# Performance work log

Measured on AMD Instinct MI355X. Metric: run time of the kernel, lower is better.

The kernel has to match this reference:

```python
import jax, jax.numpy as jnp
import numpy as np

B, C, N = 8, 256, 4096
K = C // 4  # projection dim for F and G (feat_dim // 4)


def setup_inputs() -> dict:
    key = jax.random.key(0)
    k1, k2, k3, k4, k5, k6 = jax.random.split(key, 6)
    inp = {
        "input": jax.random.normal(k1, (B, C, N), dtype=jnp.float32),
        "nms_feat": jax.random.normal(k2, (B, C, N), dtype=jnp.float32),
        "WF": jax.random.normal(k3, (K, C), dtype=jnp.float32) * (1.0 / np.sqrt(C)),
        "WG": jax.random.normal(k4, (K, C), dtype=jnp.float32) * (1.0 / np.sqrt(C)),
        "WH": jax.random.normal(k5, (C, C), dtype=jnp.float32) * (1.0 / np.sqrt(C)),
        "gamma": jax.random.normal(k6, (1,), dtype=jnp.float32),
    }
    return inp


def reference(input, nms_feat, WF, WG, WH, gamma):
    feat = nms_feat  # [B, C, N]; module uses nms_feat when provided
    b, c, n = feat.shape
    # 1x1 conv projections == channel matmuls; outputs laid out as [B, N, d]
    f = jnp.einsum('kc,bcn->bnk', WF, feat)   # [B, N, K]
    g = jnp.einsum('kc,bcn->bnk', WG, feat)   # [B, N, K]
    h = jnp.einsum('dc,bcn->bnd', WH, feat)   # [B, N, C]
    # attention scores (no scaling in original module)
    s = jnp.einsum('bnk,bmk->bnm', g, f)      # [B, N, N]
    beta = jax.nn.softmax(s, axis=-1)
    o = jnp.einsum('bnm,bmd->bnd', beta, h)   # [B, N, C]
    # NOTE: the original does a raw reshape [B,N,C] -> [B,C,N] (not a transpose);
    # we reproduce that exactly.
    o = o.reshape(b, c, n)
    return gamma * o + input
```

## Files before the change

kernel.cpp:

```cpp
#include <hip/hip_runtime.h>
#include <hip/hip_bf16.h>

#define BB 8
#define CC 256
#define NN 4096
#define KP 64
#define LOG2E 1.44269504088896f

typedef _Float16 f16x8 __attribute__((ext_vector_type(8)));
typedef _Float16 f16x4 __attribute__((ext_vector_type(4)));
typedef float    f32x4 __attribute__((ext_vector_type(4)));

#define MFMA16(a, b, c) __builtin_amdgcn_mfma_f32_16x16x32_f16((a), (b), (c), 0, 0, 0)

__device__ __forceinline__ float fast_exp2(float x) {
#if __has_builtin(__builtin_amdgcn_exp2f)
    return __builtin_amdgcn_exp2f(x);
#else
    return __expf(x * 0.69314718055994531f);
#endif
}

template<int CTRL>
__device__ __forceinline__ float dpp_ror_f(float x) {
    return __int_as_float(__builtin_amdgcn_update_dpp(
        0, __float_as_int(x), CTRL, 0xF, 0xF, true));
}
__device__ __forceinline__ float max16(float x) {
    x = fmaxf(x, dpp_ror_f<0x128>(x));
    x = fmaxf(x, dpp_ror_f<0x124>(x));
    x = fmaxf(x, dpp_ror_f<0x122>(x));
    x = fmaxf(x, dpp_ror_f<0x121>(x));
    return x;
}
__device__ __forceinline__ float sum16(float x) {
    x += dpp_ror_f<0x128>(x);
    x += dpp_ror_f<0x124>(x);
    x += dpp_ror_f<0x122>(x);
    x += dpp_ror_f<0x121>(x);
    return x;
}

__global__ __launch_bounds__(256) void wconv_kernel(
    const float* __restrict__ WF, const float* __restrict__ WG,
    const float* __restrict__ WH, _Float16* __restrict__ W16)
{
    int gid = blockIdx.x * 256 + threadIdx.x;
    int i4  = gid * 4;
    const float* src;
    if (i4 < 64 * CC)        src = WF + i4;
    else if (i4 < 128 * CC)  src = WG + (i4 - 64 * CC);
    else                     src = WH + (i4 - 128 * CC);
    float4 v = *(const float4*)src;
    f16x4 o = { (_Float16)v.x, (_Float16)v.y, (_Float16)v.z, (_Float16)v.w };
    *(f16x4*)(W16 + i4) = o;
}

__global__ __launch_bounds__(256, 3) void proj16_kernel(
    const float* __restrict__ feat, const _Float16* __restrict__ W16,
    _Float16* __restrict__ fb, _Float16* __restrict__ gb,
    _Float16* __restrict__ hT)
{
    __shared__ __align__(16) _Float16 ft[64][264];
    const int b = blockIdx.y, n0 = blockIdx.x * 64, t = threadIdx.x;

    #pragma unroll
    for (int i = 0; i < 16; i++) {
        int v = t + i * 256, c = v >> 4, nq = v & 15;
        float4 x = *(const float4*)(feat + ((size_t)b * CC + c) * NN + n0 + nq * 4);
        ft[nq * 4 + 0][c] = (_Float16)x.x;
        ft[nq * 4 + 1][c] = (_Float16)x.y;
        ft[nq * 4 + 2][c] = (_Float16)x.z;
        ft[nq * 4 + 3][c] = (_Float16)x.w;
    }
    __syncthreads();

    const int w = t >> 6, lane = t & 63, quad = lane >> 4, ln = lane & 15;
    const int rowbase = w * 96;

    f32x4 acc[6][4] = {};
    #pragma unroll
    for (int ks = 0; ks < 8; ks++) {
        const int c0 = ks * 32;
        f16x8 bfr[4];
        #pragma unroll
        for (int tf = 0; tf < 4; tf++)
            bfr[tf] = *(const f16x8*)&ft[tf * 16 + ln][c0 + quad * 8];
        #pragma unroll
        for (int af = 0; af < 6; af++) {
            f16x8 a = *(const f16x8*)(W16 + (size_t)(rowbase + af * 16 + ln) * CC + c0 + quad * 8);
            #pragma unroll
            for (int tf = 0; tf < 4; tf++)
                acc[af][tf] = MFMA16(a, bfr[tf], acc[af][tf]);
        }
    }

    #pragma unroll
    for (int af = 0; af < 6; af++) {
        const int orow0 = rowbase + af * 16 + quad * 4;
        if (orow0 < 64) {
            #pragma unroll
            for (int tf = 0; tf < 4; tf++) {
                const int tok = n0 + tf * 16 + ln;
                f16x4 pk = { (_Float16)acc[af][tf][0], (_Float16)acc[af][tf][1],
                             (_Float16)acc[af][tf][2], (_Float16)acc[af][tf][3] };
                *(f16x4*)(fb + ((size_t)b * NN + tok) * KP + orow0) = pk;
            }
        } else if (orow0 < 128) {
            #pragma unroll
            for (int tf = 0; tf < 4; tf++) {
                const int tok = n0 + tf * 16 + ln;
                f16x4 pk = { (_Float16)(acc[af][tf][0] * LOG2E),
                             (_Float16)(acc[af][tf][1] * LOG2E),
                             (_Float16)(acc[af][tf][2] * LOG2E),
                             (_Float16)(acc[af][tf][3] * LOG2E) };
                *(f16x4*)(gb + ((size_t)b * NN + tok) * KP + (orow0 - 64)) = pk;
            }
        } else {
            #pragma unroll
            for (int r = 0; r < 4; r++) {
                const int d = orow0 - 128 + r;
                f16x4 pk = { (_Float16)acc[af][0][r], (_Float16)acc[af][1][r],
                             (_Float16)acc[af][2][r], (_Float16)acc[af][3][r] };
                *(f16x4*)(hT + ((size_t)b * CC + d) * NN + n0 + ln * 4) = pk;
            }
        }
    }
}

__global__ __launch_bounds__(256, 2) void attn16_kernel(
    const _Float16* __restrict__ fb, const _Float16* __restrict__ gb,
    const _Float16* __restrict__ hT, const float* __restrict__ inp,
    const float* __restrict__ gamma, float* __restrict__ out)
{
    __shared__ __align__(16) _Float16 g_s[64][72];
    __shared__ __align__(16) _Float16 f_s[2][64][72];
    __shared__ __align__(16) _Float16 p_s[2][64][72];
    __shared__ float alpha_s[2][64];
    __shared__ float chg_s[2][4];
    __shared__ float l_s[64];

    const int b = blockIdx.x, q0 = blockIdx.y * 64, t = threadIdx.x;
    const int w = t >> 6, lane = t & 63, quad = lane >> 4, ln = lane & 15;
    const int row = t >> 2, kq = t & 3;
    const int dbase = w * 64;

    {
        const _Float16* src = gb + ((size_t)b * NN + q0 + row) * KP + kq * 16;
        *(f16x8*)&g_s[row][kq * 16]     = *(const f16x8*)(src);
        *(f16x8*)&g_s[row][kq * 16 + 8] = *(const f16x8*)(src + 8);
    }
    f16x8 fr0, fr1;
    {
        const _Float16* src = fb + ((size_t)b * NN + row) * KP + kq * 16;
        fr0 = *(const f16x8*)(src);
        fr1 = *(const f16x8*)(src + 8);
    }
    __syncthreads();

    f16x8 ag[2];
    ag[0] = *(const f16x8*)&g_s[w * 16 + ln][quad * 8];
    ag[1] = *(const f16x8*)&g_s[w * 16 + ln][32 + quad * 8];

    *(f16x8*)&f_s[0][row][kq * 16]     = fr0;
    *(f16x8*)&f_s[0][row][kq * 16 + 8] = fr1;

    f16x8 hvA[2][4], hvB[2][4];
    #pragma unroll
    for (int ks = 0; ks < 2; ks++)
        #pragma unroll
        for (int df = 0; df < 4; df++)
            hvA[ks][df] = *(const f16x8*)(hT +
                ((size_t)b * CC + dbase + df * 16 + ln) * NN + ks * 32 + quad * 8);
    {
        const _Float16* src = fb + ((size_t)b * NN + 64 + row) * KP + kq * 16;
        fr0 = *(const f16x8*)(src);
        fr1 = *(const f16x8*)(src + 8);
    }
    __syncthreads();

    float m_run[4] = {-1e30f, -1e30f, -1e30f, -1e30f};
    float l_run[4] = {0.f, 0.f, 0.f, 0.f};
    f32x4 acc[4][4] = {};

#define ATTN_PHASE(CUR, NXT, HVC, HVN, MT)                                     \
    {                                                                          \
        f32x4 S[4] = {};                                                       \
        _Pragma("unroll")                                                      \
        for (int ks = 0; ks < 2; ks++) {                                       \
            _Pragma("unroll")                                                  \
            for (int mf = 0; mf < 4; mf++) {                                   \
                f16x8 bf = *(const f16x8*)&f_s[CUR][mf * 16 + ln][ks * 32 + quad * 8]; \
                S[mf] = MFMA16(ag[ks], bf, S[mf]);                             \
            }                                                                  \
        }                                                                      \
        float pmax[4]; bool upd = false;                                       \
        _Pragma("unroll")                                                      \
        for (int r = 0; r < 4; r++) {                                          \
            pmax[r] = fmaxf(fmaxf(S[0][r], S[1][r]), fmaxf(S[2][r], S[3][r])); \
            upd |= (pmax[r] > m_run[r] + 10.0f);                               \
        }                                                                      \
        const bool wave_upd = (__ballot(upd) != 0ull);                         \
        if (wave_upd) {                                                        \
            _Pragma("unroll")                                                  \
            for (int r = 0; r < 4; r++) {                                      \
                float mx   = max16(pmax[r]);                                   \
                float mnew = fmaxf(m_run[r], mx);                              \
                float al   = fast_exp2(m_run[r] - mnew);                       \
                l_run[r] *= al;                                                \
                m_run[r]  = mnew;                                              \
                if (ln == 0) alpha_s[CUR][w * 16 + quad * 4 + r] = al;         \
            }                                                                  \
        }                                                                      \
        if (lane == 0) chg_s[CUR][w] = wave_upd ? 1.0f : 0.0f;                 \
        _Pragma("unroll")                                                      \
        for (int r = 0; r < 4; r++) {                                          \
            float p0 = fast_exp2(S[0][r] - m_run[r]);                          \
            float p1 = fast_exp2(S[1][r] - m_run[r]);                          \
            float p2 = fast_exp2(S[2][r] - m_run[r]);                          \
            float p3 = fast_exp2(S[3][r] - m_run[r]);                          \
            l_run[r] += (p0 + p1) + (p2 + p3);                                 \
            f16x4 pk = { (_Float16)p0, (_Float16)p1, (_Float16)p2, (_Float16)p3 }; \
            *(f16x4*)&p_s[CUR][w * 16 + quad * 4 + r][ln * 4] = pk;            \
        }                                                                      \
        *(f16x8*)&f_s[NXT][row][kq * 16]     = fr0;                            \
        *(f16x8*)&f_s[NXT][row][kq * 16 + 8] = fr1;                            \
        __syncthreads();                                                       \
        {                                                                      \
            const int m0n = (((MT) + 1) & 63) * 64;                            \
            _Pragma("unroll")                                                  \
            for (int ks = 0; ks < 2; ks++)                                     \
                _Pragma("unroll")                                              \
                for (int df = 0; df < 4; df++)                                 \
                    HVN[ks][df] = *(const f16x8*)(hT +                         \
                        ((size_t)b * CC + dbase + df * 16 + ln) * NN + m0n + ks * 32 + quad * 8); \
            const int m0n2 = (((MT) + 2) & 63) * 64;                           \
            const _Float16* srcf = fb + ((size_t)b * NN + m0n2 + row) * KP + kq * 16; \
            fr0 = *(const f16x8*)(srcf);                                       \
            fr1 = *(const f16x8*)(srcf + 8);                                   \
        }                                                                      \
        {                                                                      \
            float chg[4] = { chg_s[CUR][0], chg_s[CUR][1],                     \
                             chg_s[CUR][2], chg_s[CUR][3] };                   \
            _Pragma("unroll")                                                  \
            for (int qf = 0; qf < 4; qf++) {                                   \
                if (chg[qf] != 0.0f) {                                         \
                    _Pragma("unroll")                                          \
                    for (int r = 0; r < 4; r++) {                              \
                        float al = alpha_s[CUR][qf * 16 + quad * 4 + r];       \
                        _Pragma("unroll")                                      \
                        for (int df = 0; df < 4; df++)                         \
                            acc[qf][df][r] *= al;                              \
                    }                                                          \
                }                                                              \
            }                                                                  \
        }                                                                      \
        _Pragma("unroll")                                                      \
        for (int ks = 0; ks < 2; ks++) {                                       \
            _Pragma("unroll")                                                  \
            for (int qf = 0; qf < 4; qf++) {                                   \
                f16x8 ap = *(const f16x8*)&p_s[CUR][qf * 16 + ln][ks * 32 + quad * 8]; \
                _Pragma("unroll")                                              \
                for (int df = 0; df < 4; df++)                                 \
                    acc[qf][df] = MFMA16(ap, HVC[ks][df], acc[qf][df]);        \
            }                                                                  \
        }                                                                      \
    }

    #pragma unroll 1
    for (int mt2 = 0; mt2 < NN / 128; mt2++) {
        ATTN_PHASE(0, 1, hvA, hvB, mt2 * 2)
        ATTN_PHASE(1, 0, hvB, hvA, mt2 * 2 + 1)
    }
#undef ATTN_PHASE

    #pragma unroll
    for (int r = 0; r < 4; r++) {
        float lt = sum16(l_run[r]);
        if (ln == 0) l_s[w * 16 + quad * 4 + r] = lt;
    }
    __syncthreads();

    const float gam = gamma[0];
    #pragma unroll
    for (int qf = 0; qf < 4; qf++) {
        #pragma unroll
        for (int r = 0; r < 4; r++) {
            const int q = qf * 16 + quad * 4 + r;
            const float linv = 1.0f / l_s[q];
            #pragma unroll
            for (int df = 0; df < 4; df++) {
                const int d = dbase + df * 16 + ln;
                size_t idx = ((size_t)b * NN + q0 + q) * CC + d;
                out[idx] = fmaf(gam, acc[qf][df][r] * linv, inp[idx]);
            }
        }
    }
}

extern "C" void kernel_launch(void* const* d_in, const int* in_sizes, int n_in,
                              void* d_out, int out_size, void* d_ws, size_t ws_size,
                              hipStream_t stream) {
    const float* input = (const float*)d_in[0];
    const float* nms   = (const float*)d_in[1];
    const float* WF    = (const float*)d_in[2];
    const float* WG    = (const float*)d_in[3];
    const float* WH    = (const float*)d_in[4];
    const float* gamma = (const float*)d_in[5];
    float* out = (float*)d_out;

    char* ws = (char*)d_ws;
    _Float16* W16  = (_Float16*)ws;
    _Float16* fb16 = (_Float16*)(ws + 196608);
    _Float16* gb16 = (_Float16*)(ws + 196608 + 4194304);
    _Float16* hT16 = (_Float16*)(ws + 196608 + 2 * 4194304);

    wconv_kernel<<<96, 256, 0, stream>>>(WF, WG, WH, W16);
    proj16_kernel<<<dim3(NN / 64, BB), 256, 0, stream>>>(nms, W16, fb16, gb16, hT16);
    attn16_kernel<<<dim3(BB, NN / 64), 256, 0, stream>>>(fb16, gb16, hT16, input, gamma, out);
}
```

Baseline: 264.8 us.

## Load F tiles directly into registers and drop LDS staging for F and G

The attention kernel now reads the G query fragment and each F key tile straight from global memory into MFMA operand registers, so the shared-memory buffers for f and g and their store/load round trip are removed. The next F tile is prefetched right after the score MFMAs. H fragments are now loaded at the start of each phase, no longer double-buffered one phase ahead. The barrier is replaced by a custom s_waitcnt lgkmcnt plus s_barrier that skips waiting on outstanding global loads. This cuts LDS traffic and LDS footprint, but every wave now fetches F redundantly from global/L2, and H loads are exposed with less prefetch distance.

```diff
diff --git a/kernel.cpp b/kernel.cpp
--- a/kernel.cpp
+++ b/kernel.cpp
@@ -19,6 +19,12 @@
 #else
     return __expf(x * 0.69314718055994531f);
 #endif
+}
+
+__device__ __forceinline__ void barrier_lgkm() {
+    asm volatile("s_waitcnt lgkmcnt(0)" ::: "memory");
+    __builtin_amdgcn_s_barrier();
+    asm volatile("" ::: "memory");
 }
 
 template<int CTRL>
@@ -133,66 +139,58 @@
     const _Float16* __restrict__ hT, const float* __restrict__ inp,
     const float* __restrict__ gamma, float* __restrict__ out)
 {
-    __shared__ __align__(16) _Float16 g_s[64][72];
-    __shared__ __align__(16) _Float16 f_s[2][64][72];
     __shared__ __align__(16) _Float16 p_s[2][64][72];
     __shared__ float alpha_s[2][64];
+    __shared__ float l_s[64];
     __shared__ float chg_s[2][4];
-    __shared__ float l_s[64];
 
     const int b = blockIdx.x, q0 = blockIdx.y * 64, t = threadIdx.x;
     const int w = t >> 6, lane = t & 63, quad = lane >> 4, ln = lane & 15;
-    const int row = t >> 2, kq = t & 3;
     const int dbase = w * 64;
 
+    f16x8 ag[2];
     {
-        const _Float16* src = gb + ((size_t)b * NN + q0 + row) * KP + kq * 16;
-        *(f16x8*)&g_s[row][kq * 16]     = *(const f16x8*)(src);
-        *(f16x8*)&g_s[row][kq * 16 + 8] = *(const f16x8*)(src + 8);
-    }
-    f16x8 fr0, fr1;
-    {
-        const _Float16* src = fb + ((size_t)b * NN + row) * KP + kq * 16;
-        fr0 = *(const f16x8*)(src);
-        fr1 = *(const f16x8*)(src + 8);
-    }
-    __syncthreads();
-
-    f16x8 ag[2];
-    ag[0] = *(const f16x8*)&g_s[w * 16 + ln][quad * 8];
-    ag[1] = *(const f16x8*)&g_s[w * 16 + ln][32 + quad * 8];
-
-    *(f16x8*)&f_s[0][row][kq * 16]     = fr0;
-    *(f16x8*)&f_s[0][row][kq * 16 + 8] = fr1;
-
-    f16x8 hvA[2][4], hvB[2][4];
+        const _Float16* src = gb + ((size_t)b * NN + q0 + w * 16 + ln) * KP + quad * 8;
+        ag[0] = *(const f16x8*)(src);
+        ag[1] = *(const f16x8*)(src + 32);
+    }
+    f16x8 bf[2][4];
     #pragma unroll
     for (int ks = 0; ks < 2; ks++)
         #pragma unroll
-        for (int df = 0; df < 4; df++)
-            hvA[ks][df] = *(const f16x8*)(hT +
-                ((size_t)b * CC + dbase + df * 16 + ln) * NN + ks * 32 + quad * 8);
-    {
-        const _Float16* src = fb + ((size_t)b * NN + 64 + row) * KP + kq * 16;
-        fr0 = *(const f16x8*)(src);
-        fr1 = *(const f16x8*)(src + 8);
-    }
-    __syncthreads();
+        for (int mf = 0; mf < 4; mf++)
+            bf[ks][mf] = *(const f16x8*)(fb +
+                ((size_t)b * NN + mf * 16 + ln) * KP + ks * 32 + quad * 8);
 
     float m_run[4] = {-1e30f, -1e30f, -1e30f, -1e30f};
     float l_run[4] = {0.f, 0.f, 0.f, 0.f};
     f32x4 acc[4][4] = {};
-
-#define ATTN_PHASE(CUR, NXT, HVC, HVN, MT)                                     \
+    f16x8 hv[2][4];
+
+#define ATTN_PHASE(BUF, MT)                                                    \
     {                                                                          \
+        const int m0 = (MT) * 64;                                              \
+        _Pragma("unroll")                                                      \
+        for (int ks = 0; ks < 2; ks++)                                         \
+            _Pragma("unroll")                                                  \
+            for (int df = 0; df < 4; df++)                                     \
+                hv[ks][df] = *(const f16x8*)(hT +                              \
+                    ((size_t)b * CC + dbase + df * 16 + ln) * NN + m0 + ks * 32 + quad * 8); \
         f32x4 S[4] = {};                                                       \
         _Pragma("unroll")                                                      \
         for (int ks = 0; ks < 2; ks++) {                                       \
             _Pragma("unroll")                                                  \
-            for (int mf = 0; mf < 4; mf++) {                                   \
-                f16x8 bf = *(const f16x8*)&f_s[CUR][mf * 16 + ln][ks * 32 + quad * 8]; \
-                S[mf] = MFMA16(ag[ks], bf, S[mf]);                             \
-            }                                                                  \
+            for (int mf = 0; mf < 4; mf++)                                     \
+                S[mf] = MFMA16(ag[ks], bf[ks][mf], S[mf]);                     \
+        }                                                                      \
+        {                                                                      \
+            const int m0n = (((MT) + 1) & 63) * 64;        \
+            _Pragma("unroll")                                                  \
+            for (int ks = 0; ks < 2; ks++)                                     \
+                _Pragma("unroll")                                              \
+                for (int mf = 0; mf < 4; mf++)                                 \
+                    bf[ks][mf] = *(const f16x8*)(fb +                          \
+                        ((size_t)b * NN + m0n + mf * 16 + ln) * KP + ks * 32 + quad * 8); \
         }                                                                      \
         float pmax[4]; bool upd = false;                                       \
         _Pragma("unroll")                                                      \
@@ -209,10 +207,10 @@
                 float al   = fast_exp2(m_run[r] - mnew);                       \
                 l_run[r] *= al;                                                \
                 m_run[r]  = mnew;                                              \
-                if (ln == 0) alpha_s[CUR][w * 16 + quad * 4 + r] = al;         \
+                if (ln == 0) alpha_s[BUF][w * 16 + quad * 4 + r] = al;         \
             }                                                                  \
         }                                                                      \
-        if (lane == 0) chg_s[CUR][w] = wave_upd ? 1.0f : 0.0f;                 \
+        if (lane == 0) chg_s[BUF][w] = wave_upd ? 1.0f : 0.0f;                 \
         _Pragma("unroll")                                                      \
         for (int r = 0; r < 4; r++) {                                          \
             float p0 = fast_exp2(S[0][r] - m_run[r]);                          \
@@ -221,33 +219,18 @@
             float p3 = fast_exp2(S[3][r] - m_run[r]);                          \
             l_run[r] += (p0 + p1) + (p2 + p3);                                 \
             f16x4 pk = { (_Float16)p0, (_Float16)p1, (_Float16)p2, (_Float16)p3 }; \
-            *(f16x4*)&p_s[CUR][w * 16 + quad * 4 + r][ln * 4] = pk;            \
-        }                                                                      \
-        *(f16x8*)&f_s[NXT][row][kq * 16]     = fr0;                            \
-        *(f16x8*)&f_s[NXT][row][kq * 16 + 8] = fr1;                            \
-        __syncthreads();                                                       \
+            *(f16x4*)&p_s[BUF][w * 16 + quad * 4 + r][ln * 4] = pk;            \
+        }                                                                      \
+        barrier_lgkm();                                                        \
         {                                                                      \
-            const int m0n = (((MT) + 1) & 63) * 64;                            \
-            _Pragma("unroll")                                                  \
-            for (int ks = 0; ks < 2; ks++)                                     \
-                _Pragma("unroll")                                              \
-                for (int df = 0; df < 4; df++)                                 \
-                    HVN[ks][df] = *(const f16x8*)(hT +                         \
-                        ((size_t)b * CC + dbase + df * 16 + ln) * NN + m0n + ks * 32 + quad * 8); \
-            const int m0n2 = (((MT) + 2) & 63) * 64;                           \
-            const _Float16* srcf = fb + ((size_t)b * NN + m0n2 + row) * KP + kq * 16; \
-            fr0 = *(const f16x8*)(srcf);                                       \
-            fr1 = *(const f16x8*)(srcf + 8);                                   \
-        }                                                                      \
-        {                                                                      \
-            float chg[4] = { chg_s[CUR][0], chg_s[CUR][1],                     \
-                             chg_s[CUR][2], chg_s[CUR][3] };                   \
+            float chg[4] = { chg_s[BUF][0], chg_s[BUF][1],                     \
+                             chg_s[BUF][2], chg_s[BUF][3] };                   \
             _Pragma("unroll")                                                  \
             for (int qf = 0; qf < 4; qf++) {                                   \
                 if (chg[qf] != 0.0f) {                                         \
                     _Pragma("unroll")                                          \
                     for (int r = 0; r < 4; r++) {                              \
-                        float al = alpha_s[CUR][qf * 16 + quad * 4 + r];       \
+                        float al = alpha_s[BUF][qf * 16 + quad * 4 + r];       \
                         _Pragma("unroll")                                      \
                         for (int df = 0; df < 4; df++)                         \
                             acc[qf][df][r] *= al;                              \
@@ -259,18 +242,18 @@
         for (int ks = 0; ks < 2; ks++) {                                       \
             _Pragma("unroll")                                                  \
             for (int qf = 0; qf < 4; qf++) {                                   \
-                f16x8 ap = *(const f16x8*)&p_s[CUR][qf * 16 + ln][ks * 32 + quad * 8]; \
+                f16x8 ap = *(const f16x8*)&p_s[BUF][qf * 16 + ln][ks * 32 + quad * 8]; \
                 _Pragma("unroll")                                              \
                 for (int df = 0; df < 4; df++)                                 \
-                    acc[qf][df] = MFMA16(ap, HVC[ks][df], acc[qf][df]);        \
+                    acc[qf][df] = MFMA16(ap, hv[ks][df], acc[qf][df]);         \
             }                                                                  \
         }                                                                      \
     }
 
     #pragma unroll 1
     for (int mt2 = 0; mt2 < NN / 128; mt2++) {
-        ATTN_PHASE(0, 1, hvA, hvB, mt2 * 2)
-        ATTN_PHASE(1, 0, hvB, hvA, mt2 * 2 + 1)
+        ATTN_PHASE(0, mt2 * 2)
+        ATTN_PHASE(1, mt2 * 2 + 1)
     }
 #undef ATTN_PHASE
 
@@ -317,5 +300,6 @@
 
     wconv_kernel<<<96, 256, 0, stream>>>(WF, WG, WH, W16);
     proj16_kernel<<<dim3(NN / 64, BB), 256, 0, stream>>>(nms, W16, fb16, gb16, hT16);
-    attn16_kernel<<<dim3(BB, NN / 64), 256, 0, stream>>>(fb16, gb16, hT16, input, gamma, out);
-}
+    attn16_kernel<<<dim3(BB, NN / 64), 256, 0, stream>>>(
+        fb16, gb16, hT16, input, gamma, out);
+}
```

Measured after the change: 357.0 us. 34.8% more time.
